# Kernel optimization log

Hardware: AMD Instinct MI355X
Metric: run time of the kernel (lower is better)

## Reference

```python
import jax, jax.numpy as jnp
import numpy as np

B, S, C, L = 8, 256, 4, 256
E, H, NL, NS = 256, 8, 2, 8
DH = E // H
EPS = 1e-5


def _conv1d(x, w, b):
    # x: [B, Cin, L], w: [Cout, Cin, K] -> [B, Cout, L] (SAME padding, stride 1)
    y = jax.lax.conv_general_dilated(x, w, (1,), 'SAME', dimension_numbers=('NCH', 'OIH', 'NCH'))
    return y + b[None, :, None]


def _local_cnn(xs, w1, b1, w2, b2):
    # xs: [B, 4, L] for one segment; per-segment weights
    h = jax.nn.relu(_conv1d(xs, w1, b1))
    h = jax.nn.relu(_conv1d(h, w2, b2))
    return jnp.max(h, axis=-1)  # AdaptiveMaxPool1d(1) + squeeze -> [B, E]


def _layernorm(x, g, b):
    m = jnp.mean(x, axis=-1, keepdims=True)
    v = jnp.mean((x - m) ** 2, axis=-1, keepdims=True)
    return (x - m) / jnp.sqrt(v + EPS) * g + b


def setup_inputs() -> dict:
    key = jax.random.key(0)
    ks = jax.random.split(key, 24)
    n = lambda k, shp, s: jax.random.normal(k, shp, jnp.float32) * s
    return {
        'x': jax.random.normal(ks[0], (B, S, C, L), jnp.float32),
        'conv1_w': n(ks[1], (S, 128, 4, 3), 0.1), 'conv1_b': jnp.zeros((S, 128), jnp.float32),
        'conv2_w': n(ks[2], (S, E, 128, 3), 0.05), 'conv2_b': jnp.zeros((S, E), jnp.float32),
        'ln1_g': jnp.ones((NL, E), jnp.float32), 'ln1_b': jnp.zeros((NL, E), jnp.float32),
        'wq': n(ks[3], (NL, E, E), 0.02), 'bq': jnp.zeros((NL, E), jnp.float32),
        'wk': n(ks[4], (NL, E, E), 0.02), 'bk': jnp.zeros((NL, E), jnp.float32),
        'wv': n(ks[5], (NL, E, E), 0.02), 'bv': jnp.zeros((NL, E), jnp.float32),
        'wo': n(ks[6], (NL, E, E), 0.02), 'bo': jnp.zeros((NL, E), jnp.float32),
        'bias_w': n(ks[7], (NL, 4, H), 0.1), 'bias_b': jnp.zeros((NL, H), jnp.float32),
        'ln2_g': jnp.ones((NL, E), jnp.float32), 'ln2_b': jnp.zeros((NL, E), jnp.float32),
        'ffn_w1': n(ks[8], (NL, E, 2 * E), 0.02), 'ffn_b1': jnp.zeros((NL, 2 * E), jnp.float32),
        'ffn_w2': n(ks[9], (NL, 2 * E, E), 0.02), 'ffn_b2': jnp.zeros((NL, E), jnp.float32),
        'fc_w': n(ks[10], (NS * E, 2), 0.02), 'fc_b': jnp.zeros((2,), jnp.float32),
    }


def _forward(x, conv1_w, conv1_b, conv2_w, conv2_b, ln1_g, ln1_b,
             wq, bq, wk, bk, wv, bv, wo, bo, bias_w, bias_b,
             ln2_g, ln2_b, ffn_w1, ffn_b1, ffn_w2, ffn_b2, fc_w, fc_b):
    # Per-segment CNNs (vmap over segment axis with per-segment weights) -> [B, S, E]
    cnn = jax.vmap(_local_cnn, in_axes=(1, 0, 0, 0, 0), out_axes=1)(x, conv1_w, conv1_b, conv2_w, conv2_b)
    feat = _layernorm(cnn, jnp.ones((E,), cnn.dtype), jnp.zeros((E,), cnn.dtype))  # F.layer_norm, no affine

    # bias matrices: cdist (p=2), global-max normalized; positional distance; inverses
    sq = jnp.sum(feat * feat, axis=-1)  # [B, S]
    d2 = sq[:, :, None] + sq[:, None, :] - 2.0 * jnp.einsum('bie,bje->bij', feat, feat)
    dist = jnp.sqrt(jnp.maximum(d2, 0.0))
    dist = dist / (jnp.max(dist) + 1e-6)
    idx = jnp.arange(S, dtype=feat.dtype)
    rdist = jnp.abs(idx[:, None] - idx[None, :]) / (S - 1)
    rdist = jnp.broadcast_to(rdist[None], (feat.shape[0], S, S))
    attn_bias = jnp.stack([dist, rdist, 1.0 - rdist, 1.0 - dist], axis=-1)  # [B,S,S,4]

    h = feat
    scale = 1.0 / jnp.sqrt(jnp.asarray(DH, h.dtype))
    for l in range(NL):
        hn = _layernorm(h, ln1_g[l], ln1_b[l])
        q = (hn @ wq[l] + bq[l]).reshape(-1, S, H, DH)
        k = (hn @ wk[l] + bk[l]).reshape(-1, S, H, DH)
        v = (hn @ wv[l] + bv[l]).reshape(-1, S, H, DH)
        scores = jnp.einsum('bihd,bjhd->bhij', q, k) * scale
        scores = scores + jnp.einsum('bijc,ch->bhij', attn_bias, bias_w[l]) + bias_b[l][None, :, None, None]
        a = jax.nn.softmax(scores, axis=-1)
        o = jnp.einsum('bhij,bjhd->bihd', a, v).reshape(-1, S, E) @ wo[l] + bo[l]
        h = h + o
        hn2 = _layernorm(h, ln2_g[l], ln2_b[l])
        f = jax.nn.relu(hn2 @ ffn_w1[l] + ffn_b1[l]) @ ffn_w2[l] + ffn_b2[l]
        h = h + f

    # split into NS chunks along segments, max-pool each, concat (S % NS == 0)
    pooled = jnp.max(h.reshape(-1, NS, S // NS, E), axis=2).reshape(-1, NS * E)
    return pooled @ fc_w + fc_b  # [B, num_classes]


def reference(x, conv1_w, conv1_b, conv2_w, conv2_b, ln1_g, ln1_b,
              wq, bq, wk, bk, wv, bv, wo, bo, bias_w, bias_b,
              ln2_g, ln2_b, ffn_w1, ffn_b1, ffn_w2, ffn_b2, fc_w, fc_b):
    return _forward(x, conv1_w, conv1_b, conv2_w, conv2_b, ln1_g, ln1_b,
                    wq, bq, wk, bk, wv, bv, wo, bo, bias_w, bias_b,
                    ln2_g, ln2_b, ffn_w1, ffn_b1, ffn_w2, ffn_b2, fc_w, fc_b)
```

## Files before the change

### kernel.cpp

```cpp
#include <hip/hip_runtime.h>
#include <hip/hip_bf16.h>


typedef float floatx4 __attribute__((ext_vector_type(4)));
typedef short bf16x8 __attribute__((ext_vector_type(8)));

__device__ __forceinline__ float wave_sum(float v) {
    v += __shfl_xor(v, 32); v += __shfl_xor(v, 16); v += __shfl_xor(v, 8);
    v += __shfl_xor(v, 4);  v += __shfl_xor(v, 2);  v += __shfl_xor(v, 1);
    return v;
}
__device__ __forceinline__ float wave_max(float v) {
    v = fmaxf(v, __shfl_xor(v, 32)); v = fmaxf(v, __shfl_xor(v, 16));
    v = fmaxf(v, __shfl_xor(v, 8));  v = fmaxf(v, __shfl_xor(v, 4));
    v = fmaxf(v, __shfl_xor(v, 2));  v = fmaxf(v, __shfl_xor(v, 1));
    return v;
}
__device__ __forceinline__ unsigned short f2bf(float v) {
    unsigned b = __float_as_uint(v);
    unsigned r = (b + 0x7fffu + ((b >> 16) & 1u)) >> 16;
    return (unsigned short)r;
}

typedef const __attribute__((address_space(1))) unsigned int* gas_u32p;
typedef __attribute__((address_space(3))) unsigned int* las_u32p;

__device__ __forceinline__ void stage_chunk(const unsigned short* gbase,
                                            unsigned short* lbase,
                                            int wv, int lane)
{
    const char* g = (const char*)gbase + (wv << 11) + (lane << 4);
    char* l = (char*)lbase + (wv << 11);
    __builtin_amdgcn_global_load_lds((gas_u32p)(const void*)g,
                                     (las_u32p)(void*)l, 16, 0, 0);
    __builtin_amdgcn_global_load_lds((gas_u32p)(const void*)(g + 1024),
                                     (las_u32p)(void*)(l + 1024), 16, 0, 0);
}

__global__ void init_kernel(unsigned* dmax, unsigned* cnnmax) {
    const size_t i = (size_t)blockIdx.x * 256 + threadIdx.x;
    cnnmax[i] = 0u;
    if (i == 0) *dmax = 0u;
}

__global__ __launch_bounds__(256) void prep_w2_kernel(
    const float* __restrict__ w2, unsigned short* __restrict__ w2b)
{
    const int s = blockIdx.x;
    const int part = blockIdx.y;
    const float* src = w2 + (size_t)s * 98304;
    unsigned short* dst = w2b + (size_t)s * 98304;
    for (int o = part * 24576 + threadIdx.x; o < (part + 1) * 24576; o += 256) {
        const int c  = o >> 13;
        const int w  = o & 8191;
        const int co = w >> 5;
        const int up = (w >> 3) & 3;
        const int t  = w & 7;
        const int u  = (up ^ co ^ (co >> 2)) & 3;
        const int kk = c * 32 + u * 8 + t;
        const int ci = kk & 127, tap = kk >> 7;
        dst[o] = f2bf(src[(size_t)co * 384 + ci * 3 + tap]);
    }
}

__global__ __launch_bounds__(512, 4) void conv2_fused_kernel(
    const unsigned short* __restrict__ w2b,
    const float* __restrict__ x,
    const float* __restrict__ w1,
    const float* __restrict__ b1,
    const float* __restrict__ b2,
    unsigned* __restrict__ cnnmax)
{
    __shared__ float xs[4][258];
    __shared__ float w1s[1536];
    __shared__ unsigned short Hs[130 * 136];
    __shared__ unsigned short Ab[2][8192];

    const int tid = threadIdx.x;
    const int lane = tid & 63;
    const int wv = __builtin_amdgcn_readfirstlane((int)(tid >> 6));
    const int wm = wv & 3, wn = wv >> 2;
    const int s = blockIdx.x;
    const int nt = blockIdx.y;
    const int b = nt >> 1;
    const int l0 = (nt & 1) * 128;
    const int lr = lane & 15;
    const int quad = lane >> 4;
    const int qk = quad * 8;

    const float* xp = x + ((size_t)(b * 256 + s)) * 1024;
    for (int i = tid; i < 1024; i += 512) {
        const int ci = i >> 8, l = i & 255;
        xs[ci][l + 1] = xp[i];
    }
    if (tid < 4) { xs[tid][0] = 0.f; xs[tid][257] = 0.f; }
    const float* w1p = w1 + (size_t)s * 1536;
    for (int i = tid; i < 1536; i += 512) w1s[i] = w1p[i];
    const int co1 = tid & 127;
    const float bb1 = b1[s * 128 + co1];
    __syncthreads();

    const unsigned short* wchunks = w2b + (size_t)s * 98304;
    stage_chunk(wchunks,        &Ab[0][0], wv, lane);
    stage_chunk(wchunks + 8192, &Ab[1][0], wv, lane);

    {
        const int g = tid >> 7;
        float wreg[12];
#pragma unroll
        for (int k = 0; k < 12; k++) wreg[k] = w1s[co1 * 12 + k];
        for (int pr = g; pr < 130; pr += 4) {
            const int l = l0 - 1 + pr;
            float a = 0.f;
            if ((unsigned)l < 256u) {
                a = bb1;
#pragma unroll
                for (int ci = 0; ci < 4; ci++)
#pragma unroll
                    for (int k = 0; k < 3; k++) a = fmaf(wreg[ci * 3 + k], xs[ci][l + k], a);
                a = fmaxf(a, 0.f);
            }
            Hs[pr * 136 + co1] = f2bf(a);
        }
    }
    asm volatile("s_waitcnt lgkmcnt(0)" ::: "memory");
    __builtin_amdgcn_s_barrier();

    floatx4 acc[4][4];
#pragma unroll
    for (int r = 0; r < 4; r++)
#pragma unroll
        for (int c = 0; c < 4; c++) acc[r][c] = (floatx4){0.f, 0.f, 0.f, 0.f};

    const int nb = wn * 64;
    const int aoff = wm * 2048 + lr * 32 + (((quad ^ lr ^ (lr >> 2)) & 3) * 8);
    const int hbase = (nb + lr) * 136 + qk;

#define CSTEP(KS, BUF, WAITN, DOSTAGE)                                          \
    {                                                                            \
        asm volatile("s_waitcnt vmcnt(" #WAITN ")" ::: "memory");                \
        __builtin_amdgcn_s_barrier();                                            \
        __builtin_amdgcn_sched_barrier(0);                                       \
        const int tap_ = (KS) >> 2, ci0_ = ((KS) & 3) * 32;                      \
        const unsigned short* ap = &Ab[BUF][aoff];                               \
        const unsigned short* hp = &Hs[hbase + tap_ * 136 + ci0_];               \
        bf16x8 a[4], bb[4];                                                      \
        _Pragma("unroll")                                                        \
        for (int r = 0; r < 4; r++) a[r] = *(const bf16x8*)(ap + r * 512);       \
        _Pragma("unroll")                                                        \
        for (int c = 0; c < 4; c++) bb[c] = *(const bf16x8*)(hp + c * 2176);     \
        _Pragma("unroll")                                                        \
        for (int r = 0; r < 4; r++)                                              \
            _Pragma("unroll")                                                    \
            for (int c = 0; c < 4; c++)                                          \
                acc[r][c] = __builtin_amdgcn_mfma_f32_16x16x32_bf16(             \
                    a[r], bb[c], acc[r][c], 0, 0, 0);                            \
        __builtin_amdgcn_sched_barrier(0);                                       \
        __builtin_amdgcn_s_barrier();                                            \
        __builtin_amdgcn_sched_barrier(0);                                       \
        if (DOSTAGE)                                                             \
            stage_chunk(wchunks + ((KS) + 2) * 8192, &Ab[BUF][0], wv, lane);     \
    }

    for (int kp = 0; kp < 5; kp++) {
        const int ks = kp * 2;
        CSTEP(ks,     0, 2, 1);
        CSTEP(ks + 1, 1, 2, 1);
    }
    CSTEP(10, 0, 2, 0);
    CSTEP(11, 1, 0, 0);
#undef CSTEP

    const float* b2s = b2 + s * 256;
    unsigned* cmrow = cnnmax + ((size_t)(b * 256 + s)) * 256;
#pragma unroll
    for (int r = 0; r < 4; r++) {
#pragma unroll
        for (int e = 0; e < 4; e++) {
            const int co = wm * 64 + r * 16 + quad * 4 + e;
            const float bias = b2s[co];
            float mv = 0.f;
#pragma unroll
            for (int c = 0; c < 4; c++) mv = fmaxf(mv, acc[r][c][e] + bias);
            mv = fmaxf(mv, __shfl_xor(mv, 1));
            mv = fmaxf(mv, __shfl_xor(mv, 2));
            mv = fmaxf(mv, __shfl_xor(mv, 4));
            mv = fmaxf(mv, __shfl_xor(mv, 8));
            if (lr == 0) atomicMax(&cmrow[co], __float_as_uint(mv));
        }
    }
}

__global__ __launch_bounds__(256) void ln0_kernel(
    const unsigned* __restrict__ cm, float* __restrict__ out, float* __restrict__ sqv)
{
    const int tid = threadIdx.x, lane = tid & 63, wid = tid >> 6;
    const int row = blockIdx.x * 4 + wid;
    const unsigned* xr = cm + (size_t)row * 256;
    float v[4];
#pragma unroll
    for (int i = 0; i < 4; i++) v[i] = __uint_as_float(xr[lane + 64 * i]);
    float sm = wave_sum(v[0] + v[1] + v[2] + v[3]);
    const float mean = sm * (1.f / 256.f);
    float qv = 0.f;
#pragma unroll
    for (int i = 0; i < 4; i++) { const float d = v[i] - mean; qv = fmaf(d, d, qv); }
    qv = wave_sum(qv);
    const float inv = rsqrtf(qv * (1.f / 256.f) + 1e-5f);
    float* orow = out + (size_t)row * 256;
#pragma unroll
    for (int i = 0; i < 4; i++) orow[lane + 64 * i] = (v[i] - mean) * inv;
    if (lane == 0) sqv[row] = qv * inv * inv;
}

__global__ __launch_bounds__(256) void dist_kernel(
    const float* __restrict__ feat, const float* __restrict__ sq,
    float* __restrict__ dist, unsigned* __restrict__ dmax)
{
    __shared__ float Fi[32][260];
    __shared__ float Fj[16][260];
    __shared__ float redm[4];
    const int tid = threadIdx.x;
    const int bid = blockIdx.x;
    const int b = bid >> 7, it = (bid >> 4) & 7, jt = bid & 15;
    const float* fb = feat + (size_t)b * 65536;
    for (int idx = tid; idx < 32 * 256; idx += 256) {
        const int r = idx >> 8, e = idx & 255;
        Fi[r][e] = fb[(it * 32 + r) * 256 + e];
    }
    for (int idx = tid; idx < 16 * 256; idx += 256) {
        const int r = idx >> 8, e = idx & 255;
        Fj[r][e] = fb[(jt * 16 + r) * 256 + e];
    }
    __syncthreads();
    const int ii = tid >> 3, j0 = (tid & 7) * 2;
    float acc[2] = {0.f, 0.f};
    for (int e = 0; e < 256; e += 4) {
        const float4 a = *(const float4*)&Fi[ii][e];
#pragma unroll
        for (int u = 0; u < 2; u++) {
            const float4 bv = *(const float4*)&Fj[j0 + u][e];
            acc[u] += a.x * bv.x + a.y * bv.y + a.z * bv.z + a.w * bv.w;
        }
    }
    const float sqi = sq[b * 256 + it * 32 + ii];
    float mymax = 0.f;
#pragma unroll
    for (int u = 0; u < 2; u++) {
        const float d2 = sqi + sq[b * 256 + jt * 16 + j0 + u] - 2.f * acc[u];
        const float d = sqrtf(fmaxf(d2, 0.f));
        dist[((size_t)b * 256 + it * 32 + ii) * 256 + jt * 16 + j0 + u] = d;
        mymax = fmaxf(mymax, d);
    }
    mymax = wave_max(mymax);
    if ((tid & 63) == 0) redm[tid >> 6] = mymax;
    __syncthreads();
    if (tid == 0) {
        const float m = fmaxf(fmaxf(redm[0], redm[1]), fmaxf(redm[2], redm[3]));
        atomicMax(dmax, __float_as_uint(m));
    }
}

__global__ __launch_bounds__(256) void ln_bf_kernel(
    const float* __restrict__ x, const float* __restrict__ g, const float* __restrict__ bta,
    unsigned short* __restrict__ out)
{
    const int tid = threadIdx.x, lane = tid & 63, wid = tid >> 6;
    const int row = blockIdx.x * 4 + wid;
    const float* xr = x + (size_t)row * 256;
    float v[4];
#pragma unroll
    for (int i = 0; i < 4; i++) v[i] = xr[lane + 64 * i];
    float sm = wave_sum(v[0] + v[1] + v[2] + v[3]);
    const float mean = sm * (1.f / 256.f);
    float q = 0.f;
#pragma unroll
    for (int i = 0; i < 4; i++) { const float d = v[i] - mean; q = fmaf(d, d, q); }
    q = wave_sum(q);
    const float inv = rsqrtf(q * (1.f / 256.f) + 1e-5f);
    unsigned short* orow = out + (size_t)row * 256;
#pragma unroll
    for (int i = 0; i < 4; i++) {
        const int e = lane + 64 * i;
        orow[e] = f2bf((v[i] - mean) * inv * g[e] + bta[e]);
    }
}

__global__ __launch_bounds__(256) void prep_wt_kernel(
    const float* __restrict__ wq, const float* __restrict__ wk, const float* __restrict__ wv,
    const float* __restrict__ wo, const float* __restrict__ f1, const float* __restrict__ f2,
    unsigned short* __restrict__ wtb)
{
    __shared__ float t[32][33];
    const int z = blockIdx.z;
    const int l = z / 6, id = z % 6;
    const float* src; int K_, N_; size_t doff;
    switch (id) {
        case 0:  src = wq + (size_t)l * 65536;  K_ = 256; N_ = 256; doff = 0;      break;
        case 1:  src = wk + (size_t)l * 65536;  K_ = 256; N_ = 256; doff = 65536;  break;
        case 2:  src = wv + (size_t)l * 65536;  K_ = 256; N_ = 256; doff = 131072; break;
        case 3:  src = wo + (size_t)l * 65536;  K_ = 256; N_ = 256; doff = 196608; break;
        case 4:  src = f1 + (size_t)l * 131072; K_ = 256; N_ = 512; doff = 262144; break;
        default: src = f2 + (size_t)l * 131072; K_ = 512; N_ = 256; doff = 393216; break;
    }
    const int k0 = blockIdx.x * 32, n0 = blockIdx.y * 32;
    if (k0 >= K_ || n0 >= N_) return;
    unsigned short* dst = wtb + (size_t)l * 524288 + doff;
    const int c = threadIdx.x & 31, rq = threadIdx.x >> 5;
#pragma unroll
    for (int i = 0; i < 4; i++) {
        const int r = rq + i * 8;
        t[r][c] = src[(size_t)(k0 + r) * N_ + n0 + c];
    }
    __syncthreads();
#pragma unroll
    for (int i = 0; i < 4; i++) {
        const int r = rq + i * 8;
        dst[(size_t)(n0 + r) * K_ + k0 + c] = f2bf(t[c][r]);
    }
}

__global__ __launch_bounds__(128) void gemm_mfma_kernel(
    const unsigned short* __restrict__ A, const unsigned short* __restrict__ Wt,
    const float* __restrict__ b0, const float* __restrict__ b1, const float* __restrict__ b2,
    const float* __restrict__ R, float* __restrict__ outf,
    unsigned short* __restrict__ o0, unsigned short* __restrict__ o1, unsigned short* __restrict__ o2,
    int K, int mode)
{
    const int tid = threadIdx.x;
    const int lane = tid & 63, lr = lane & 15, quad = lane >> 4;
    const int wv = __builtin_amdgcn_readfirstlane((int)(tid >> 6));
    const int m0 = blockIdx.x * 128 + wv * 64;
    const int n0 = blockIdx.y * 32;

    floatx4 acc[4][2];
#pragma unroll
    for (int r = 0; r < 4; r++)
#pragma unroll
        for (int c = 0; c < 2; c++) acc[r][c] = (floatx4){0.f, 0.f, 0.f, 0.f};

    const unsigned short* Ap = A + (size_t)(m0 + lr) * K + quad * 8;
    const unsigned short* Bp = Wt + (size_t)(n0 + lr) * K + quad * 8;
    const int nks = K >> 5;
#pragma unroll 4
    for (int ks = 0; ks < nks; ks++) {
        const int ko = ks * 32;
        bf16x8 a[4], b[2];
#pragma unroll
        for (int r = 0; r < 4; r++) a[r] = *(const bf16x8*)(Ap + (size_t)r * 16 * K + ko);
#pragma unroll
        for (int c = 0; c < 2; c++) b[c] = *(const bf16x8*)(Bp + (size_t)c * 16 * K + ko);
#pragma unroll
        for (int r = 0; r < 4; r++)
#pragma unroll
            for (int c = 0; c < 2; c++)
                acc[r][c] = __builtin_amdgcn_mfma_f32_16x16x32_bf16(a[r], b[c], acc[r][c], 0, 0, 0);
    }

    if (mode == 0) {
        const int which = n0 >> 8, nn0 = n0 & 255;
        if (which < 2) {
            unsigned short* op = which ? o1 : o0;
            const float* bp = which ? b1 : b0;
#pragma unroll
            for (int r = 0; r < 4; r++)
#pragma unroll
                for (int c = 0; c < 2; c++)
#pragma unroll
                    for (int e = 0; e < 4; e++) {
                        const int m = m0 + r * 16 + quad * 4 + e;
                        const int n = nn0 + c * 16 + lr;
                        op[(size_t)m * 256 + n] = f2bf(acc[r][c][e] + bp[n]);
                    }
        } else {
#pragma unroll
            for (int r = 0; r < 4; r++)
#pragma unroll
                for (int c = 0; c < 2; c++)
#pragma unroll
                    for (int e = 0; e < 4; e++) {
                        const int m = m0 + r * 16 + quad * 4 + e;
                        const int nn = nn0 + c * 16 + lr;
                        const int bb_ = m >> 8, j = m & 255, hh = nn >> 5, d = nn & 31;
                        o2[(size_t)((bb_ * 8 + hh) * 32 + d) * 256 + j] = f2bf(acc[r][c][e] + b2[nn]);
                    }
        }
    } else if (mode == 1) {
#pragma unroll
        for (int r = 0; r < 4; r++)
#pragma unroll
            for (int c = 0; c < 2; c++)
#pragma unroll
                for (int e = 0; e < 4; e++) {
                    const int m = m0 + r * 16 + quad * 4 + e;
                    const int n = n0 + c * 16 + lr;
                    outf[(size_t)m * 256 + n] = acc[r][c][e] + b0[n] + R[(size_t)m * 256 + n];
                }
    } else {
#pragma unroll
        for (int r = 0; r < 4; r++)
#pragma unroll
            for (int c = 0; c < 2; c++)
#pragma unroll
                for (int e = 0; e < 4; e++) {
                    const int m = m0 + r * 16 + quad * 4 + e;
                    const int n = n0 + c * 16 + lr;
                    o0[(size_t)m * 512 + n] = f2bf(fmaxf(acc[r][c][e] + b0[n], 0.f));
                }
    }
}

__global__ __launch_bounds__(256) void attn_mfma_kernel(
    const unsigned short* __restrict__ q_bf, const unsigned short* __restrict__ k_bf,
    const unsigned short* __restrict__ vt_bf,
    const float* __restrict__ dist, const unsigned* __restrict__ dmax,
    const float* __restrict__ bw, const float* __restrict__ bb,
    unsigned short* __restrict__ ao_bf)
{
    __shared__ unsigned short Ps[4][16][264];
    const int tid = threadIdx.x;
    const int lane = tid & 63, lr = lane & 15, quad = lane >> 4;
    const int wv = __builtin_amdgcn_readfirstlane((int)(tid >> 6));
    const int ic = blockIdx.x, hh = blockIdx.y, b = blockIdx.z;
    const int i0 = ic * 64 + wv * 16;

    const float dinv = 1.f / (__uint_as_float(*dmax) + 1e-6f);
    const float w0 = bw[0 * 8 + hh], w1 = bw[1 * 8 + hh], w2 = bw[2 * 8 + hh], w3 = bw[3 * 8 + hh];
    const float bbh = bb[hh];
    const float scale = 0.17677669529663687f;

    const bf16x8 aq = *(const bf16x8*)(q_bf + (size_t)(b * 256 + i0 + lr) * 256 + hh * 32 + quad * 8);
    floatx4 sc[16];
#pragma unroll
    for (int c = 0; c < 16; c++) {
        const bf16x8 bk = *(const bf16x8*)(k_bf + (size_t)(b * 256 + c * 16 + lr) * 256 + hh * 32 + quad * 8);
        sc[c] = __builtin_amdgcn_mfma_f32_16x16x32_bf16(aq, bk, (floatx4){0.f, 0.f, 0.f, 0.f}, 0, 0, 0);
    }

#pragma unroll
    for (int e = 0; e < 4; e++) {
        const int i = i0 + quad * 4 + e;
        const float* drow = dist + ((size_t)(b * 256 + i)) * 256;
        float bs[16];
        float mx = -1e30f;
#pragma unroll
        for (int c = 0; c < 16; c++) {
            const int j = c * 16 + lr;
            const float dn = drow[j] * dinv;
            const float rd = fabsf((float)(i - j)) * (1.f / 255.f);
            bs[c] = sc[c][e] * scale + w0 * dn + w1 * rd + w2 * (1.f - rd) + w3 * (1.f - dn) + bbh;
            mx = fmaxf(mx, bs[c]);
        }
        mx = fmaxf(mx, __shfl_xor(mx, 1)); mx = fmaxf(mx, __shfl_xor(mx, 2));
        mx = fmaxf(mx, __shfl_xor(mx, 4)); mx = fmaxf(mx, __shfl_xor(mx, 8));
        float sm = 0.f;
#pragma unroll
        for (int c = 0; c < 16; c++) { bs[c] = __expf(bs[c] - mx); sm += bs[c]; }
        sm += __shfl_xor(sm, 1); sm += __shfl_xor(sm, 2);
        sm += __shfl_xor(sm, 4); sm += __shfl_xor(sm, 8);
        const float rs = 1.f / sm;
#pragma unroll
        for (int c = 0; c < 16; c++)
            Ps[wv][quad * 4 + e][c * 16 + lr] = f2bf(bs[c] * rs);
    }
    __syncthreads();

    floatx4 oc[2];
    oc[0] = (floatx4){0.f, 0.f, 0.f, 0.f};
    oc[1] = (floatx4){0.f, 0.f, 0.f, 0.f};
    const unsigned short* vtb = vt_bf + (size_t)(b * 8 + hh) * 8192;
#pragma unroll
    for (int ks = 0; ks < 8; ks++) {
        const bf16x8 ap = *(const bf16x8*)(&Ps[wv][lr][ks * 32 + quad * 8]);
#pragma unroll
        for (int c2 = 0; c2 < 2; c2++) {
            const bf16x8 bvv = *(const bf16x8*)(vtb + (size_t)(c2 * 16 + lr) * 256 + ks * 32 + quad * 8);
            oc[c2] = __builtin_amdgcn_mfma_f32_16x16x32_bf16(ap, bvv, oc[c2], 0, 0, 0);
        }
    }
#pragma unroll
    for (int c2 = 0; c2 < 2; c2++)
#pragma unroll
        for (int e = 0; e < 4; e++)
            ao_bf[(size_t)(b * 256 + i0 + quad * 4 + e) * 256 + hh * 32 + c2 * 16 + lr] = f2bf(oc[c2][e]);
}

__global__ __launch_bounds__(256) void pool_fc_kernel(
    const float* __restrict__ h, const float* __restrict__ fcw,
    const float* __restrict__ fcb, float* __restrict__ out)
{
    __shared__ float red[8];
    const int b = blockIdx.x, tid = threadIdx.x, lane = tid & 63, wid = tid >> 6;
    float a0 = 0.f, a1 = 0.f;
    for (int ns = 0; ns < 8; ns++) {
        const float* hp = h + ((size_t)(b * 256 + ns * 32)) * 256 + tid;
        float m = hp[0];
#pragma unroll
        for (int r = 1; r < 32; r++) m = fmaxf(m, hp[(size_t)r * 256]);
        a0 = fmaf(m, fcw[(ns * 256 + tid) * 2 + 0], a0);
        a1 = fmaf(m, fcw[(ns * 256 + tid) * 2 + 1], a1);
    }
    a0 = wave_sum(a0);
    a1 = wave_sum(a1);
    if (lane == 0) { red[wid] = a0; red[4 + wid] = a1; }
    __syncthreads();
    if (tid == 0) out[b * 2 + 0] = red[0] + red[1] + red[2] + red[3] + fcb[0];
    if (tid == 1) out[b * 2 + 1] = red[4] + red[5] + red[6] + red[7] + fcb[1];
}

extern "C" void kernel_launch(void* const* d_in, const int* in_sizes, int n_in,
                              void* d_out, int out_size, void* d_ws, size_t ws_size,
                              hipStream_t stream)
{
    (void)in_sizes; (void)n_in; (void)out_size; (void)ws_size;
    const float* x       = (const float*)d_in[0];
    const float* conv1_w = (const float*)d_in[1];
    const float* conv1_b = (const float*)d_in[2];
    const float* conv2_w = (const float*)d_in[3];
    const float* conv2_b = (const float*)d_in[4];
    const float* ln1_g   = (const float*)d_in[5];
    const float* ln1_b   = (const float*)d_in[6];
    const float* wq = (const float*)d_in[7];  const float* bq = (const float*)d_in[8];
    const float* wk = (const float*)d_in[9];  const float* bk = (const float*)d_in[10];
    const float* wvp = (const float*)d_in[11]; const float* bv = (const float*)d_in[12];
    const float* wo = (const float*)d_in[13]; const float* bo = (const float*)d_in[14];
    const float* bias_w = (const float*)d_in[15];
    const float* bias_b = (const float*)d_in[16];
    const float* ln2_g  = (const float*)d_in[17];
    const float* ln2_b  = (const float*)d_in[18];
    const float* ffn_w1 = (const float*)d_in[19]; const float* ffn_b1 = (const float*)d_in[20];
    const float* ffn_w2 = (const float*)d_in[21]; const float* ffn_b2 = (const float*)d_in[22];
    const float* fc_w   = (const float*)d_in[23]; const float* fc_b = (const float*)d_in[24];
    float* out = (float*)d_out;

    float* ws = (float*)d_ws;
    float* h    = ws;
    float* dist = h + 524288;
    float* sqv  = dist + 524288;
    unsigned* dmax = (unsigned*)(sqv + 2048);
    unsigned* cnnmax = (unsigned*)(sqv + 2048 + 16);
    unsigned short* hn_bf = (unsigned short*)(sqv + 2048 + 16 + 524288);
    unsigned short* q_bf  = hn_bf + 524288;
    unsigned short* k_bf  = q_bf + 524288;
    unsigned short* vt_bf = k_bf + 524288;
    unsigned short* ao_bf = vt_bf + 524288;
    unsigned short* fm_bf = ao_bf + 524288;
    unsigned short* wtb   = fm_bf + 1048576;
    unsigned short* w2b   = wtb + 1048576;

    init_kernel<<<2048, 256, 0, stream>>>(dmax, cnnmax);
    prep_wt_kernel<<<dim3(16, 16, 12), 256, 0, stream>>>(wq, wk, wvp, wo, ffn_w1, ffn_w2, wtb);
    prep_w2_kernel<<<dim3(256, 4), 256, 0, stream>>>(conv2_w, w2b);
    conv2_fused_kernel<<<dim3(256, 16), 512, 0, stream>>>(
        w2b, x, conv1_w, conv1_b, conv2_b, cnnmax);
    ln0_kernel<<<512, 256, 0, stream>>>(cnnmax, h, sqv);
    dist_kernel<<<1024, 256, 0, stream>>>(h, sqv, dist, dmax);

    for (int l = 0; l < 2; l++) {
        const unsigned short* wqkvT = wtb + (size_t)l * 524288;
        const unsigned short* woT   = wqkvT + 196608;
        const unsigned short* f1T   = wqkvT + 262144;
        const unsigned short* f2T   = wqkvT + 393216;

        ln_bf_kernel<<<512, 256, 0, stream>>>(h, ln1_g + l * 256, ln1_b + l * 256, hn_bf);
        gemm_mfma_kernel<<<dim3(16, 24), 128, 0, stream>>>(
            hn_bf, wqkvT, bq + l * 256, bk + l * 256, bv + l * 256,
            nullptr, nullptr, q_bf, k_bf, vt_bf, 256, 0);
        attn_mfma_kernel<<<dim3(4, 8, 8), 256, 0, stream>>>(
            q_bf, k_bf, vt_bf, dist, dmax, bias_w + l * 32, bias_b + l * 8, ao_bf);
        gemm_mfma_kernel<<<dim3(16, 8), 128, 0, stream>>>(
            ao_bf, woT, bo + l * 256, nullptr, nullptr,
            h, h, nullptr, nullptr, nullptr, 256, 1);
        ln_bf_kernel<<<512, 256, 0, stream>>>(h, ln2_g + l * 256, ln2_b + l * 256, hn_bf);
        gemm_mfma_kernel<<<dim3(16, 16), 128, 0, stream>>>(
            hn_bf, f1T, ffn_b1 + l * 512, nullptr, nullptr,
            nullptr, nullptr, fm_bf, nullptr, nullptr, 256, 2);
        gemm_mfma_kernel<<<dim3(16, 8), 128, 0, stream>>>(
            fm_bf, f2T, ffn_b2 + l * 256, nullptr, nullptr,
            h, h, nullptr, nullptr, nullptr, 512, 1);
    }
    pool_fc_kernel<<<8, 256, 0, stream>>>(h, fc_w, fc_b, out);
}
```

Before: 576.8 us.

## Remap conv2 blocks per XCD for weight L2 reuse and restructure K-loop pipeline

Flattens the conv2 grid to 1D and remaps block IDs so that all 16 batch/half tiles of a segment, and consecutive segments, land on the same XCD. The segment's conv2 weights are then reused from that XCD's L2 rather than fetched by several XCDs. The K loop is also rewritten to single-chunk lookahead: it issues the next chunk's stage right after the barrier and waits vmcnt(0) each step, replacing the two-deep prefetch with one barrier per step. The shallower prefetch may expose more global load latency per step.

```diff
diff --git a/kernel.cpp b/kernel.cpp
--- a/kernel.cpp
+++ b/kernel.cpp
@@ -80,8 +80,11 @@
     const int lane = tid & 63;
     const int wv = __builtin_amdgcn_readfirstlane((int)(tid >> 6));
     const int wm = wv & 3, wn = wv >> 2;
-    const int s = blockIdx.x;
-    const int nt = blockIdx.y;
+    const int bid = blockIdx.x;
+    const int xcd = bid & 7;
+    const int pos = bid >> 3;
+    const int s   = xcd * 32 + (pos >> 4);
+    const int nt  = pos & 15;
     const int b = nt >> 1;
     const int l0 = (nt & 1) * 128;
     const int lr = lane & 15;
@@ -101,8 +104,7 @@
     __syncthreads();
 
     const unsigned short* wchunks = w2b + (size_t)s * 98304;
-    stage_chunk(wchunks,        &Ab[0][0], wv, lane);
-    stage_chunk(wchunks + 8192, &Ab[1][0], wv, lane);
+    stage_chunk(wchunks, &Ab[0][0], wv, lane);
 
     {
         const int g = tid >> 7;
@@ -123,8 +125,6 @@
             Hs[pr * 136 + co1] = f2bf(a);
         }
     }
-    asm volatile("s_waitcnt lgkmcnt(0)" ::: "memory");
-    __builtin_amdgcn_s_barrier();
 
     floatx4 acc[4][4];
 #pragma unroll
@@ -136,40 +136,34 @@
     const int aoff = wm * 2048 + lr * 32 + (((quad ^ lr ^ (lr >> 2)) & 3) * 8);
     const int hbase = (nb + lr) * 136 + qk;
 
-#define CSTEP(KS, BUF, WAITN, DOSTAGE)                                          \
-    {                                                                            \
-        asm volatile("s_waitcnt vmcnt(" #WAITN ")" ::: "memory");                \
-        __builtin_amdgcn_s_barrier();                                            \
-        __builtin_amdgcn_sched_barrier(0);                                       \
-        const int tap_ = (KS) >> 2, ci0_ = ((KS) & 3) * 32;                      \
-        const unsigned short* ap = &Ab[BUF][aoff];                               \
-        const unsigned short* hp = &Hs[hbase + tap_ * 136 + ci0_];               \
-        bf16x8 a[4], bb[4];                                                      \
-        _Pragma("unroll")                                                        \
-        for (int r = 0; r < 4; r++) a[r] = *(const bf16x8*)(ap + r * 512);       \
-        _Pragma("unroll")                                                        \
-        for (int c = 0; c < 4; c++) bb[c] = *(const bf16x8*)(hp + c * 2176);     \
-        _Pragma("unroll")                                                        \
-        for (int r = 0; r < 4; r++)                                              \
-            _Pragma("unroll")                                                    \
-            for (int c = 0; c < 4; c++)                                          \
-                acc[r][c] = __builtin_amdgcn_mfma_f32_16x16x32_bf16(             \
-                    a[r], bb[c], acc[r][c], 0, 0, 0);                            \
-        __builtin_amdgcn_sched_barrier(0);                                       \
-        __builtin_amdgcn_s_barrier();                                            \
-        __builtin_amdgcn_sched_barrier(0);                                       \
-        if (DOSTAGE)                                                             \
-            stage_chunk(wchunks + ((KS) + 2) * 8192, &Ab[BUF][0], wv, lane);     \
-    }
-
-    for (int kp = 0; kp < 5; kp++) {
-        const int ks = kp * 2;
-        CSTEP(ks,     0, 2, 1);
-        CSTEP(ks + 1, 1, 2, 1);
-    }
-    CSTEP(10, 0, 2, 0);
-    CSTEP(11, 1, 0, 0);
-#undef CSTEP
+    asm volatile("s_waitcnt vmcnt(0) lgkmcnt(0)" ::: "memory");
+    __builtin_amdgcn_s_barrier();
+    __builtin_amdgcn_sched_barrier(0);
+
+#pragma unroll
+    for (int ks = 0; ks < 12; ks++) {
+        if (ks) {
+            asm volatile("s_waitcnt vmcnt(0)" ::: "memory");
+            __builtin_amdgcn_s_barrier();
+            __builtin_amdgcn_sched_barrier(0);
+        }
+        if (ks < 11)
+            stage_chunk(wchunks + (size_t)(ks + 1) * 8192, &Ab[(ks + 1) & 1][0], wv, lane);
+        const int tap_ = ks >> 2, ci0_ = (ks & 3) * 32;
+        const unsigned short* ap = &Ab[ks & 1][aoff];
+        const unsigned short* hp = &Hs[hbase + tap_ * 136 + ci0_];
+        bf16x8 a[4], bb[4];
+#pragma unroll
+        for (int r = 0; r < 4; r++) a[r] = *(const bf16x8*)(ap + r * 512);
+#pragma unroll
+        for (int c = 0; c < 4; c++) bb[c] = *(const bf16x8*)(hp + c * 2176);
+#pragma unroll
+        for (int r = 0; r < 4; r++)
+#pragma unroll
+            for (int c = 0; c < 4; c++)
+                acc[r][c] = __builtin_amdgcn_mfma_f32_16x16x32_bf16(
+                    a[r], bb[c], acc[r][c], 0, 0, 0);
+    }
 
     const float* b2s = b2 + s * 256;
     unsigned* cmrow = cnnmax + ((size_t)(b * 256 + s)) * 256;
@@ -551,7 +545,7 @@
     init_kernel<<<2048, 256, 0, stream>>>(dmax, cnnmax);
     prep_wt_kernel<<<dim3(16, 16, 12), 256, 0, stream>>>(wq, wk, wvp, wo, ffn_w1, ffn_w2, wtb);
     prep_w2_kernel<<<dim3(256, 4), 256, 0, stream>>>(conv2_w, w2b);
-    conv2_fused_kernel<<<dim3(256, 16), 512, 0, stream>>>(
+    conv2_fused_kernel<<<4096, 512, 0, stream>>>(
         w2b, x, conv1_w, conv1_b, conv2_b, cnnmax);
     ln0_kernel<<<512, 256, 0, stream>>>(cnnmax, h, sqv);
     dist_kernel<<<1024, 256, 0, stream>>>(h, sqv, dist, dmax);
```

Result: no change. 568.2 us (-1.5%).
